# Kernel tuning notes

Hardware: AMD Instinct MI355X
Metric: run time of the kernel (lower is better)

## Reference

```python
import jax, jax.numpy as jnp
import numpy as np

T, G, K, N = 8192, 8, 1024, 2048

def setup_inputs() -> dict:
    key = jax.random.key(0)
    k1, k2, k3 = jax.random.split(key, 3)
    x = jax.random.normal(k1, (T, K), dtype=jnp.float32)
    w = jax.random.normal(k2, (G, N, K), dtype=jnp.float32) * 0.02
    # cumulative end-offsets per group: sorted, last entry == T (covers all tokens)
    offs = jnp.sort(jax.random.randint(k3, (G,), 0, T).astype(jnp.int32))
    offs = offs.at[-1].set(T)
    return {"input": x, "weight": w, "grouped_mm_offs": offs}

def reference(input, weight, grouped_mm_offs):
    # grouped_mm(input, weight.transpose(1,2), offs): token t in group g iff
    # offs[g-1] <= t < offs[g]; out[t] = input[t] @ weight[g].T
    t = input.shape[0]
    g = weight.shape[0]
    gid = jnp.searchsorted(grouped_mm_offs, jnp.arange(t), side="right")  # [T]
    out = jnp.zeros((t, weight.shape[1]), dtype=input.dtype)
    for gi in range(g):  # fixed small expert loop; data dims stay vectorized
        xg = jnp.where((gid == gi)[:, None], input, jnp.zeros((), input.dtype))
        out = out + xg @ weight[gi].T
    return out
```

## Files before the change

kernel.cpp:

```cpp
#include <hip/hip_runtime.h>
#include <hip/hip_bf16.h>


#define T_DIM 8192
#define G_DIM 8
#define K_DIM 1024
#define N_DIM 2048
#define MAX_PAIRS 72

using short8  = __attribute__((ext_vector_type(8))) short;
using f32x4   = __attribute__((ext_vector_type(4))) float;
using ushort8 = __attribute__((ext_vector_type(8))) unsigned short;

typedef __attribute__((address_space(1))) void gvoid;
typedef __attribute__((address_space(3))) void lvoid;

__global__ __launch_bounds__(256) void cvt_kernel(const float* __restrict__ x,
                                                  const float* __restrict__ w,
                                                  ushort8* __restrict__ xb,
                                                  ushort8* __restrict__ wb,
                                                  int n8x, int n8tot) {
  const int stride = gridDim.x * blockDim.x;
  for (int i = blockIdx.x * blockDim.x + threadIdx.x; i < n8tot; i += 2 * stride) {
#pragma unroll
    for (int u = 0; u < 2; ++u) {
      const int idx = i + u * stride;
      if (idx >= n8tot) break;
      const f32x4* s; ushort8* d; int j;
      if (idx < n8x) { s = (const f32x4*)x; d = xb; j = idx; }
      else           { s = (const f32x4*)w; d = wb; j = idx - n8x; }
      f32x4 v0 = __builtin_nontemporal_load(&s[2 * j]);
      f32x4 v1 = __builtin_nontemporal_load(&s[2 * j + 1]);
      ushort8 o;
      o[0] = __builtin_bit_cast(unsigned short, __float2bfloat16(v0[0]));
      o[1] = __builtin_bit_cast(unsigned short, __float2bfloat16(v0[1]));
      o[2] = __builtin_bit_cast(unsigned short, __float2bfloat16(v0[2]));
      o[3] = __builtin_bit_cast(unsigned short, __float2bfloat16(v0[3]));
      o[4] = __builtin_bit_cast(unsigned short, __float2bfloat16(v1[0]));
      o[5] = __builtin_bit_cast(unsigned short, __float2bfloat16(v1[1]));
      o[6] = __builtin_bit_cast(unsigned short, __float2bfloat16(v1[2]));
      o[7] = __builtin_bit_cast(unsigned short, __float2bfloat16(v1[3]));
      d[j] = o;
    }
  }
}

__global__ __launch_bounds__(256, 4) void grouped_gemm_kernel(
    const __hip_bfloat16* __restrict__ xb,
    const __hip_bfloat16* __restrict__ wb,
    const int* __restrict__ offs,
    float* __restrict__ out) {
  int offv[G_DIM];
#pragma unroll
  for (int i = 0; i < G_DIM; ++i) offv[i] = offs[i];

  const int p = blockIdx.y;
  int g = -1, tile = 0, lo = 0, hi = 0, pre = 0;
#pragma unroll
  for (int gi = 0; gi < G_DIM; ++gi) {
    const int l = gi ? offv[gi - 1] : 0;
    const int h = offv[gi];
    const int t0 = l >> 7;
    const int cnt = (h > l) ? (((h + 127) >> 7) - t0) : 0;
    if (g < 0 && p < pre + cnt) { g = gi; tile = t0 + (p - pre); lo = l; hi = h; }
    pre += cnt;
  }
  if (g < 0) return;

  const int m0 = tile * 128;
  const int n0 = blockIdx.x * 128;

  __shared__ __align__(16) __hip_bfloat16 As[128 * 64];
  __shared__ __align__(16) __hip_bfloat16 Bs[128 * 64];

  const __hip_bfloat16* wg = wb + (size_t)g * N_DIM * K_DIM;

  const int lane = threadIdx.x & 63;
  const int wid  = threadIdx.x >> 6;
  const int wm   = wid >> 1;
  const int wn   = wid & 1;

  const int srow = lane >> 3;
  const int scol = ((lane & 7) ^ srow) * 8;

  f32x4 acc[4][4] = {};

  for (int kk = 0; kk < K_DIM / 64; ++kk) {
    const int k0 = kk * 64;
#pragma unroll
    for (int i = 0; i < 4; ++i) {
      const int j   = wid * 4 + i;
      const int row = j * 8 + srow;
      const __hip_bfloat16* ga = xb + (size_t)(m0 + row) * K_DIM + k0 + scol;
      const __hip_bfloat16* gb = wg + (size_t)(n0 + row) * K_DIM + k0 + scol;
      __builtin_amdgcn_global_load_lds((gvoid*)ga, (lvoid*)(As + j * 512), 16, 0, 0);
      __builtin_amdgcn_global_load_lds((gvoid*)gb, (lvoid*)(Bs + j * 512), 16, 0, 0);
    }
    __syncthreads();

#pragma unroll
    for (int ks = 0; ks < 2; ++ks) {
      const int kb  = ks * 4 + (lane >> 4);
      const int off = ((kb ^ (lane & 7)) * 8);
      short8 a[4], b[4];
#pragma unroll
      for (int mt = 0; mt < 4; ++mt)
        a[mt] = *reinterpret_cast<const short8*>(
            As + (wm * 64 + mt * 16 + (lane & 15)) * 64 + off);
#pragma unroll
      for (int nt = 0; nt < 4; ++nt)
        b[nt] = *reinterpret_cast<const short8*>(
            Bs + (wn * 64 + nt * 16 + (lane & 15)) * 64 + off);
#pragma unroll
      for (int mt = 0; mt < 4; ++mt)
#pragma unroll
        for (int nt = 0; nt < 4; ++nt)
          acc[mt][nt] = __builtin_amdgcn_mfma_f32_16x16x32_bf16(
              a[mt], b[nt], acc[mt][nt], 0, 0, 0);
    }
    __syncthreads();
  }

  const int quad = lane >> 4;
#pragma unroll
  for (int mt = 0; mt < 4; ++mt) {
    const int rbase = m0 + wm * 64 + mt * 16 + quad * 4;
#pragma unroll
    for (int r = 0; r < 4; ++r) {
      const int row = rbase + r;
      if (row < lo || row >= hi) continue;
#pragma unroll
      for (int nt = 0; nt < 4; ++nt) {
        const int col = n0 + wn * 64 + nt * 16 + (lane & 15);
        out[(size_t)row * N_DIM + col] = acc[mt][nt][r];
      }
    }
  }
}

__global__ __launch_bounds__(256) void fallback_kernel(
    const float* __restrict__ x, const float* __restrict__ w,
    const int* __restrict__ offs, float* __restrict__ out) {
  __shared__ float xs[K_DIM];
  const int t = blockIdx.y;
  int g = 0;
  while (g < G_DIM - 1 && offs[g] <= t) ++g;
  for (int i = threadIdx.x; i < K_DIM; i += blockDim.x)
    xs[i] = x[(size_t)t * K_DIM + i];
  __syncthreads();
  const int n = blockIdx.x * blockDim.x + threadIdx.x;
  const float* wr = w + ((size_t)g * N_DIM + n) * K_DIM;
  float s = 0.f;
  for (int k = 0; k < K_DIM; ++k) s += xs[k] * wr[k];
  out[(size_t)t * N_DIM + n] = s;
}

extern "C" void kernel_launch(void* const* d_in, const int* in_sizes, int n_in,
                              void* d_out, int out_size, void* d_ws, size_t ws_size,
                              hipStream_t stream) {
  const float* x    = (const float*)d_in[0];
  const float* w    = (const float*)d_in[1];
  const int*   offs = (const int*)d_in[2];
  float*       out  = (float*)d_out;

  const size_t x_elems = (size_t)T_DIM * K_DIM;
  const size_t w_elems = (size_t)G_DIM * N_DIM * K_DIM;
  const size_t need    = (x_elems + w_elems) * sizeof(__hip_bfloat16);

  if (ws_size < need) {
    fallback_kernel<<<dim3(N_DIM / 256, T_DIM), 256, 0, stream>>>(x, w, offs, out);
    return;
  }

  __hip_bfloat16* xb = (__hip_bfloat16*)d_ws;
  __hip_bfloat16* wb = xb + x_elems;

  const int n8x   = (int)(x_elems / 8);
  const int n8tot = (int)((x_elems + w_elems) / 8);
  cvt_kernel<<<4096, 256, 0, stream>>>(x, w, (ushort8*)xb, (ushort8*)wb,
                                       n8x, n8tot);

  grouped_gemm_kernel<<<dim3(N_DIM / 128, MAX_PAIRS), 256, 0, stream>>>(
      xb, wb, offs, out);
}
```

Before: 183.9 us.

## Use 256x128 tiles with 8 waves and multi-stage LDS pipelining

Raises the GEMM block tile from 128x128 to 256x128 with 512 threads and 8 waves, and splits A and B into half-tiles held in a 4-slot LDS ring. Loads for the next k-steps are interleaved with MFMA work through explicit vmcnt waits, barriers and setprio. Block indices are remapped so that groups of blocks share the same M tile across N tiles, aiming for better L2 reuse. The aim is to hide global-load latency and reduce redundant traffic. The cost is more barriers per k-step, fragile hand-tuned waitcnt logic, and more padding waste at group boundaries.

```diff
diff --git a/kernel.cpp b/kernel.cpp
--- a/kernel.cpp
+++ b/kernel.cpp
@@ -6,7 +6,8 @@
 #define G_DIM 8
 #define K_DIM 1024
 #define N_DIM 2048
-#define MAX_PAIRS 72
+#define MAX_PAIRS 40
+#define NT (K_DIM / 64)
 
 using short8  = __attribute__((ext_vector_type(8))) short;
 using f32x4   = __attribute__((ext_vector_type(4))) float;
@@ -14,6 +15,8 @@
 
 typedef __attribute__((address_space(1))) void gvoid;
 typedef __attribute__((address_space(3))) void lvoid;
+
+#define FENCE() asm volatile("" ::: "memory")
 
 __global__ __launch_bounds__(256) void cvt_kernel(const float* __restrict__ x,
                                                   const float* __restrict__ w,
@@ -45,33 +48,38 @@
   }
 }
 
-__global__ __launch_bounds__(256, 4) void grouped_gemm_kernel(
+__global__ __launch_bounds__(512, 2) void grouped_gemm_kernel(
     const __hip_bfloat16* __restrict__ xb,
     const __hip_bfloat16* __restrict__ wb,
     const int* __restrict__ offs,
     float* __restrict__ out) {
+  const int v  = blockIdx.y * 16 + blockIdx.x;
+  const int c  = v & 7;
+  const int l  = v >> 3;
+  const int p  = c * 5 + (l % 5);
+  const int nb = l / 5;
+  const int n0 = nb * 128;
+
   int offv[G_DIM];
 #pragma unroll
   for (int i = 0; i < G_DIM; ++i) offv[i] = offs[i];
 
-  const int p = blockIdx.y;
   int g = -1, tile = 0, lo = 0, hi = 0, pre = 0;
 #pragma unroll
   for (int gi = 0; gi < G_DIM; ++gi) {
-    const int l = gi ? offv[gi - 1] : 0;
-    const int h = offv[gi];
-    const int t0 = l >> 7;
-    const int cnt = (h > l) ? (((h + 127) >> 7) - t0) : 0;
-    if (g < 0 && p < pre + cnt) { g = gi; tile = t0 + (p - pre); lo = l; hi = h; }
+    const int lb = gi ? offv[gi - 1] : 0;
+    const int hb = offv[gi];
+    const int t0 = lb >> 8;
+    const int cnt = (hb > lb) ? (((hb + 255) >> 8) - t0) : 0;
+    if (g < 0 && p < pre + cnt) { g = gi; tile = t0 + (p - pre); lo = lb; hi = hb; }
     pre += cnt;
   }
   if (g < 0) return;
 
-  const int m0 = tile * 128;
-  const int n0 = blockIdx.x * 128;
-
-  __shared__ __align__(16) __hip_bfloat16 As[128 * 64];
-  __shared__ __align__(16) __hip_bfloat16 Bs[128 * 64];
+  const int m0 = tile * 256;
+
+  __shared__ __align__(16) __hip_bfloat16 Ar[4][128 * 64];
+  __shared__ __align__(16) __hip_bfloat16 Br[4][64 * 64];
 
   const __hip_bfloat16* wg = wb + (size_t)g * N_DIM * K_DIM;
 
@@ -83,56 +91,109 @@
   const int srow = lane >> 3;
   const int scol = ((lane & 7) ^ srow) * 8;
 
+  const __hip_bfloat16* aSrc0 = xb + (size_t)(m0 + srow) * K_DIM + scol;
+  const __hip_bfloat16* bSrc0 = wg + (size_t)(n0 + srow) * K_DIM + scol;
+
+  auto stageA = [&](int tt, int hi) {
+    const int slot = (2 * tt + hi) & 3;
+#pragma unroll
+    for (int i = 0; i < 2; ++i) {
+      const int ch = wid * 2 + i;
+      const __hip_bfloat16* src = aSrc0 + (size_t)(hi * 128 + ch * 8) * K_DIM + tt * 64;
+      __builtin_amdgcn_global_load_lds((gvoid*)src,
+                                       (lvoid*)(&Ar[slot][ch * 512 + lane * 8]),
+                                       16, 0, 0);
+    }
+  };
+  auto stageB = [&](int tt, int hi) {
+    const int slot = (2 * tt + hi) & 3;
+    const __hip_bfloat16* src = bSrc0 + (size_t)(hi * 64 + wid * 8) * K_DIM + tt * 64;
+    __builtin_amdgcn_global_load_lds((gvoid*)src,
+                                     (lvoid*)(&Br[slot][wid * 512 + lane * 8]),
+                                     16, 0, 0);
+  };
+
   f32x4 acc[4][4] = {};
 
-  for (int kk = 0; kk < K_DIM / 64; ++kk) {
-    const int k0 = kk * 64;
-#pragma unroll
-    for (int i = 0; i < 4; ++i) {
-      const int j   = wid * 4 + i;
-      const int row = j * 8 + srow;
-      const __hip_bfloat16* ga = xb + (size_t)(m0 + row) * K_DIM + k0 + scol;
-      const __hip_bfloat16* gb = wg + (size_t)(n0 + row) * K_DIM + k0 + scol;
-      __builtin_amdgcn_global_load_lds((gvoid*)ga, (lvoid*)(As + j * 512), 16, 0, 0);
-      __builtin_amdgcn_global_load_lds((gvoid*)gb, (lvoid*)(Bs + j * 512), 16, 0, 0);
-    }
-    __syncthreads();
-
-#pragma unroll
-    for (int ks = 0; ks < 2; ++ks) {
-      const int kb  = ks * 4 + (lane >> 4);
-      const int off = ((kb ^ (lane & 7)) * 8);
-      short8 a[4], b[4];
-#pragma unroll
-      for (int mt = 0; mt < 4; ++mt)
-        a[mt] = *reinterpret_cast<const short8*>(
-            As + (wm * 64 + mt * 16 + (lane & 15)) * 64 + off);
-#pragma unroll
-      for (int nt = 0; nt < 4; ++nt)
-        b[nt] = *reinterpret_cast<const short8*>(
-            Bs + (wn * 64 + nt * 16 + (lane & 15)) * 64 + off);
-#pragma unroll
-      for (int mt = 0; mt < 4; ++mt)
-#pragma unroll
-        for (int nt = 0; nt < 4; ++nt)
-          acc[mt][nt] = __builtin_amdgcn_mfma_f32_16x16x32_bf16(
-              a[mt], b[nt], acc[mt][nt], 0, 0, 0);
-    }
-    __syncthreads();
+  stageA(0, 0); stageA(0, 1);
+  stageB(0, 0); stageB(0, 1);
+  stageA(1, 0); stageA(1, 1);
+  asm volatile("s_waitcnt vmcnt(4)" ::: "memory");
+  __builtin_amdgcn_s_barrier();
+  FENCE();
+
+  const int ahalf = wm >> 1;
+  const int arow0 = (wm & 1) * 64;
+
+  for (int kt = 0; kt < NT; ++kt) {
+    const int sA = (2 * kt + ahalf) & 3;
+    const int sB = (2 * kt + wn) & 3;
+    short8 a[4][2];
+
+#pragma unroll
+    for (int nf = 0; nf < 4; ++nf) {
+      if (nf == 0) {
+#pragma unroll
+        for (int mf = 0; mf < 4; ++mf)
+#pragma unroll
+          for (int ks = 0; ks < 2; ++ks) {
+            const int off = (((ks * 4 + (lane >> 4)) ^ (lane & 7)) * 8);
+            a[mf][ks] = *reinterpret_cast<const short8*>(
+                &Ar[sA][(arow0 + mf * 16 + (lane & 15)) * 64 + off]);
+          }
+      }
+      short8 b0, b1;
+      {
+        const int row = nf * 16 + (lane & 15);
+        const int o0  = (((0 * 4 + (lane >> 4)) ^ (lane & 7)) * 8);
+        const int o1  = (((1 * 4 + (lane >> 4)) ^ (lane & 7)) * 8);
+        b0 = *reinterpret_cast<const short8*>(&Br[sB][row * 64 + o0]);
+        b1 = *reinterpret_cast<const short8*>(&Br[sB][row * 64 + o1]);
+      }
+
+      if (nf == 1 && kt + 1 < NT) { stageB(kt + 1, 0); stageB(kt + 1, 1); }
+      if (nf == 2 && kt + 2 < NT) { stageA(kt + 2, 0); }
+      if (nf == 3) {
+        if (kt + 2 < NT) stageA(kt + 2, 1);
+        if (kt < NT - 2) {
+          asm volatile("s_waitcnt vmcnt(4)" ::: "memory");
+        } else {
+          asm volatile("s_waitcnt vmcnt(0)" ::: "memory");
+        }
+      }
+
+      FENCE();
+      __builtin_amdgcn_s_barrier();
+      FENCE();
+
+      __builtin_amdgcn_s_setprio(1);
+#pragma unroll
+      for (int mf = 0; mf < 4; ++mf) {
+        acc[mf][nf] = __builtin_amdgcn_mfma_f32_16x16x32_bf16(
+            a[mf][0], b0, acc[mf][nf], 0, 0, 0);
+        acc[mf][nf] = __builtin_amdgcn_mfma_f32_16x16x32_bf16(
+            a[mf][1], b1, acc[mf][nf], 0, 0, 0);
+      }
+      __builtin_amdgcn_s_setprio(0);
+
+      FENCE();
+      __builtin_amdgcn_s_barrier();
+      FENCE();
+    }
   }
 
   const int quad = lane >> 4;
 #pragma unroll
-  for (int mt = 0; mt < 4; ++mt) {
-    const int rbase = m0 + wm * 64 + mt * 16 + quad * 4;
+  for (int mf = 0; mf < 4; ++mf) {
+    const int rbase = m0 + wm * 64 + mf * 16 + quad * 4;
 #pragma unroll
     for (int r = 0; r < 4; ++r) {
       const int row = rbase + r;
       if (row < lo || row >= hi) continue;
 #pragma unroll
-      for (int nt = 0; nt < 4; ++nt) {
-        const int col = n0 + wn * 64 + nt * 16 + (lane & 15);
-        out[(size_t)row * N_DIM + col] = acc[mt][nt][r];
+      for (int nf = 0; nf < 4; ++nf) {
+        const int col = n0 + wn * 64 + nf * 16 + (lane & 15);
+        out[(size_t)row * N_DIM + col] = acc[mf][nf][r];
       }
     }
   }
@@ -180,6 +241,6 @@
   cvt_kernel<<<4096, 256, 0, stream>>>(x, w, (ushort8*)xb, (ushort8*)wb,
                                        n8x, n8tot);
 
-  grouped_gemm_kernel<<<dim3(N_DIM / 128, MAX_PAIRS), 256, 0, stream>>>(
+  grouped_gemm_kernel<<<dim3(16, MAX_PAIRS), 512, 0, stream>>>(
       xb, wb, offs, out);
 }
```

Measured after the change: 214.9 us. 16.9% more time.
